# Performance work log

Hardware: AMD Instinct MI355X
Metric: run time of the kernel (lower is better)

The kernel has to match this reference:

```python
import jax, jax.numpy as jnp
import numpy as np

EPS = 1e-12  # F.normalize eps
TEMP = 0.03


def _l2norm(x):
    # torch F.normalize: x / max(||x||, eps)
    n = jnp.sqrt(jnp.sum(x * x, axis=-1, keepdims=True))
    return x / jnp.maximum(n, EPS)


def setup_inputs() -> dict:
    key = jax.random.key(0)
    ks = jax.random.split(key, 8)
    B, C, H, W = 8, 256, 64, 64
    M = 2024
    Ch = C // 4
    s = 1.0 / np.sqrt(C)
    return {
        "feats": jax.random.normal(ks[0], (B, C, H, W), jnp.float32),
        "fg_memory": jax.random.normal(ks[1], (M, C), jnp.float32) * s,
        "bg_memory": jax.random.normal(ks[2], (M, C), jnp.float32) * s,
        "w1_fg": jax.random.normal(ks[3], (C, Ch), jnp.float32) * s,
        "b1_fg": jnp.zeros((Ch,), jnp.float32),
        "w2_fg": jax.random.normal(ks[4], (Ch, 1), jnp.float32) * (1.0 / np.sqrt(Ch)),
        "b2_fg": jnp.zeros((1,), jnp.float32),
        "w1_bg": jax.random.normal(ks[5], (C, Ch), jnp.float32) * s,
        "b1_bg": jnp.zeros((Ch,), jnp.float32),
        "w2_bg": jax.random.normal(ks[6], (Ch, 1), jnp.float32) * (1.0 / np.sqrt(Ch)),
        "b2_bg": jnp.zeros((1,), jnp.float32),
    }


def _gate(x, w1, b1, w2, b2):
    h = jax.nn.relu(x @ w1 + b1)
    return jax.nn.sigmoid(h @ w2 + b2)  # [N,1]


def reference(feats, fg_memory, bg_memory, w1_fg, b1_fg, w2_fg, b2_fg,
              w1_bg, b1_bg, w2_bg, b2_bg):
    B, C, H, W = feats.shape
    x = jnp.transpose(feats, (0, 2, 3, 1)).reshape(-1, C)  # [N,C]
    xn = _l2norm(x)
    fgn = _l2norm(fg_memory)  # [M,C]
    bgn = _l2norm(bg_memory)

    attn_fg = jax.nn.softmax((xn @ fgn.T) / TEMP, axis=1)  # [N,M]
    mem_fg = attn_fg @ fgn                                  # [N,C]
    attn_bg = jax.nn.softmax((xn @ bgn.T) / TEMP, axis=1)
    mem_bg = attn_bg @ bgn

    g_fg = _gate(xn, w1_fg, b1_fg, w2_fg, b2_fg)
    g_bg = _gate(xn, w1_bg, b1_bg, w2_bg, b2_bg)

    fused = xn + g_fg * mem_fg - g_bg * mem_bg
    return jnp.transpose(fused.reshape(B, H, W, C), (0, 3, 1, 2))
```

## Files before the change

kernel.cpp:

```cpp
#include <hip/hip_runtime.h>
#include <math.h>

#define B_   8
#define C_   256
#define HW_  4096
#define N_   32768
#define M_   2024
#define MP_  2048
#define CH_  64
#define NCHUNK (MP_ / 64)
#define INV_TEMP 33.333333333333336f
#define NEPS 1e-12f

typedef __attribute__((ext_vector_type(8))) short short8;
typedef __attribute__((ext_vector_type(4))) float floatx4;

__device__ __forceinline__ float wred64(float s) {
#pragma unroll
  for (int off = 32; off > 0; off >>= 1) s += __shfl_xor(s, off, 64);
  return s;
}

__device__ __forceinline__ unsigned short f2bf(float f) {
  union { float f; unsigned u; } v; v.f = f;
  unsigned r = v.u + 0x7FFFu + ((v.u >> 16) & 1u);
  return (unsigned short)(r >> 16);
}
__device__ __forceinline__ float bf2f(unsigned short b) {
  union { unsigned u; float f; } v; v.u = ((unsigned)b) << 16; return v.f;
}

__device__ __forceinline__ void barrier_lds_only() {
  asm volatile("s_waitcnt lgkmcnt(0)\n\ts_barrier" ::: "memory");
}

__device__ __forceinline__ void async_copy16(const unsigned short* gsrc,
                                             unsigned short* lds) {
  __builtin_amdgcn_global_load_lds(
      (const __attribute__((address_space(1))) void*)gsrc,
      (__attribute__((address_space(3))) void*)lds, 16, 0, 0);
}

__global__ __launch_bounds__(256) void norm_mem_kernel(
    const float* __restrict__ fg, const float* __restrict__ bg,
    unsigned short* __restrict__ fgS, unsigned short* __restrict__ bgS,
    unsigned short* __restrict__ fgT, unsigned short* __restrict__ bgT) {
  __shared__ unsigned short tile[64][258];
  int bid = blockIdx.x;
  const float* src; unsigned short *ms, *mt; int r0;
  if (bid < 32) { src = fg; ms = fgS; mt = fgT; r0 = bid * 64; }
  else          { src = bg; ms = bgS; mt = bgT; r0 = (bid - 32) * 64; }
  int t = threadIdx.x;
  int rr = t >> 2, c4 = t & 3;
  int row = r0 + rr;
  int chunk = r0 >> 6;
  float v[64];
  float s = 0.f;
  if (row < M_) {
    const float4* p = (const float4*)(src + (size_t)row * C_ + c4 * 64);
#pragma unroll
    for (int i = 0; i < 16; ++i) {
      float4 q = p[i];
      v[i * 4 + 0] = q.x; v[i * 4 + 1] = q.y; v[i * 4 + 2] = q.z; v[i * 4 + 3] = q.w;
      s += q.x * q.x + q.y * q.y + q.z * q.z + q.w * q.w;
    }
  } else {
#pragma unroll
    for (int i = 0; i < 64; ++i) v[i] = 0.f;
  }
  s += __shfl_xor(s, 1, 64);
  s += __shfl_xor(s, 2, 64);
  float inv = (row < M_) ? 1.0f / fmaxf(sqrtf(s), NEPS) : 0.f;
#pragma unroll
  for (int i = 0; i < 16; ++i) {
    int c = c4 * 64 + i * 4;
    ushort4 o;
    o.x = f2bf(v[i * 4 + 0] * inv); o.y = f2bf(v[i * 4 + 1] * inv);
    o.z = f2bf(v[i * 4 + 2] * inv); o.w = f2bf(v[i * 4 + 3] * inv);
    int unit = (chunk * 32 + (c >> 5) * 4 + ((c >> 3) & 3)) * 64 + rr;
    *(ushort4*)&ms[(size_t)unit * 8 + (c & 7)] = o;
    *(ushort4*)&tile[rr][c] = o;
  }
  __syncthreads();
  int m = t & 63, cw = t >> 6;
#pragma unroll 8
  for (int j = 0; j < 64; ++j) {
    int c = cw * 64 + j;
    mt[(size_t)c * MP_ + r0 + m] = tile[m][c];
  }
}

__global__ __launch_bounds__(256) void prep_x_kernel(
    const float* __restrict__ feats, float* __restrict__ invn,
    unsigned short* __restrict__ xnb) {
  __shared__ unsigned short tileb[256][66];
  __shared__ float part[4][64];
  __shared__ float invs[64];
  int t = threadIdx.x, hwl = t & 63, cw = t >> 6;
  int n0 = blockIdx.x * 64;
  int b = n0 >> 12, hw0 = n0 & 4095;
  const float* p = feats + (size_t)b * C_ * HW_ + hw0 + hwl;
  float s = 0.f;
#pragma unroll 8
  for (int i = 0; i < 64; ++i) {
    int c = cw * 64 + i;
    float v = p[(size_t)c * HW_];
    s += v * v;
    tileb[c][hwl] = f2bf(v);
  }
  part[cw][hwl] = s;
  __syncthreads();
  if (t < 64) {
    float tot = part[0][t] + part[1][t] + part[2][t] + part[3][t];
    float inv = 1.0f / fmaxf(sqrtf(tot), NEPS);
    invn[n0 + t] = inv;
    invs[t] = inv;
  }
  __syncthreads();
  int px = t >> 2, q = t & 3;
  float iv = invs[px];
  unsigned short* xp = xnb + (size_t)(n0 + px) * C_;
#pragma unroll
  for (int blk = 0; blk < 8; ++blk) {
    int cb = blk * 4 + q;
    short8 o;
#pragma unroll
    for (int j = 0; j < 8; ++j)
      o[j] = (short)f2bf(bf2f(tileb[cb * 8 + j][px]) * iv);
    *(short8*)&xp[cb * 8] = o;
  }
}

__global__ __launch_bounds__(256) void gate_kernel(
    const unsigned short* __restrict__ xnb,
    const float* __restrict__ w1f, const float* __restrict__ b1f,
    const float* __restrict__ w2f, const float* __restrict__ b2f,
    const float* __restrict__ w1b, const float* __restrict__ b1b,
    const float* __restrict__ w2b, const float* __restrict__ b2b,
    float* __restrict__ gf, float* __restrict__ gb) {
  __shared__ float xr[16][C_];
  int t = threadIdx.x, w = t >> 6, lane = t & 63;
  int n0 = blockIdx.x * 16;
#pragma unroll
  for (int pp = 0; pp < 4; ++pp) {
    int px = w * 4 + pp;
    ushort4 u = *(const ushort4*)&xnb[(size_t)(n0 + px) * C_ + lane * 4];
    xr[px][lane * 4 + 0] = bf2f(u.x);
    xr[px][lane * 4 + 1] = bf2f(u.y);
    xr[px][lane * 4 + 2] = bf2f(u.z);
    xr[px][lane * 4 + 3] = bf2f(u.w);
  }
  __syncthreads();
  float hf[4], hb[4];
#pragma unroll
  for (int pp = 0; pp < 4; ++pp) { hf[pp] = b1f[lane]; hb[pp] = b1b[lane]; }
#pragma unroll 4
  for (int c = 0; c < C_; ++c) {
    float wf = w1f[c * CH_ + lane];
    float wb = w1b[c * CH_ + lane];
#pragma unroll
    for (int pp = 0; pp < 4; ++pp) {
      float x = xr[w * 4 + pp][c];
      hf[pp] += x * wf;
      hb[pp] += x * wb;
    }
  }
  float b2fv = b2f[0], b2bv = b2b[0];
#pragma unroll
  for (int pp = 0; pp < 4; ++pp) {
    float sf = fmaxf(hf[pp], 0.f) * w2f[lane];
    float sb = fmaxf(hb[pp], 0.f) * w2b[lane];
    sf = wred64(sf);
    sb = wred64(sb);
    if (lane == 0) {
      gf[n0 + w * 4 + pp] = 1.f / (1.f + __expf(-(sf + b2fv)));
      gb[n0 + w * 4 + pp] = 1.f / (1.f + __expf(-(sb + b2bv)));
    }
  }
}

__device__ __forceinline__ void stage_chunk(const unsigned short* memS, int mc,
                                            unsigned short* mtile, int w, int l) {
  const unsigned short* src = memS + (size_t)mc * 16384;
#pragma unroll
  for (int it = 0; it < 4; ++it) {
    int seg = (it * 8 + w) * 512;
    async_copy16(src + seg + l * 8, mtile + seg);
  }
}

__global__ __launch_bounds__(512, 4) void flash_fused_kernel(
    const unsigned short* __restrict__ xnb,
    const unsigned short* __restrict__ fgS, const unsigned short* __restrict__ fgT,
    const unsigned short* __restrict__ bgS, const unsigned short* __restrict__ bgT,
    const float* __restrict__ gf, const float* __restrict__ gb,
    const float* __restrict__ feats, const float* __restrict__ invn,
    float* __restrict__ out) {
  __shared__ __align__(16) char smem[49664];
  unsigned short* mtile = (unsigned short*)smem;
  unsigned short* Pbuf0 = (unsigned short*)(smem + 32768);
  unsigned short* Pbuf1 = (unsigned short*)(smem + 40960);
  float* rowsum = (float*)(smem + 49152);
  float* comb   = (float*)(smem + 49408);
  float* trans  = (float*)smem;

  int t = threadIdx.x;
  int w = t >> 6, l = t & 63;
  int lm = l & 15, quad = l >> 4;
  int rg = w & 3, mh = w >> 2;
  int row0 = blockIdx.x * 64;

  short8 afrag[8];
  {
    const unsigned short* ap = xnb + (size_t)(row0 + 16 * rg + lm) * C_ + quad * 8;
#pragma unroll
    for (int kb = 0; kb < 8; ++kb)
      afrag[kb] = *(const short8*)(ap + kb * 32);
  }

  int bb = row0 >> 12, hw0 = row0 & 4095;
  float iv = invn[row0 + l];
  size_t ob = (size_t)bb * (size_t)C_ * HW_ + hw0 + l;

#pragma unroll 1
  for (int pass = 0; pass < 2; ++pass) {
    const unsigned short* memS  = pass ? bgS : fgS;
    const unsigned short* membT = pass ? bgT : fgT;
    const float* gp = pass ? gb : gf;

    floatx4 accO[4][2];
#pragma unroll
    for (int rt = 0; rt < 4; ++rt)
#pragma unroll
      for (int ct = 0; ct < 2; ++ct) accO[rt][ct] = (floatx4){0.f, 0.f, 0.f, 0.f};
    float rs[4] = {0.f, 0.f, 0.f, 0.f};
    if (t < 64) rowsum[t] = 0.f;

    stage_chunk(memS, 0, mtile, w, l);

#pragma unroll 1
    for (int mc = 0; mc < NCHUNK; ++mc) {
      __syncthreads();

      short8 bfT[2][2];
#pragma unroll
      for (int ct = 0; ct < 2; ++ct) {
        const unsigned short* tp =
            membT + (size_t)(w * 32 + ct * 16 + lm) * MP_ + mc * 64 + quad * 8;
        bfT[ct][0] = *(const short8*)(tp);
        bfT[ct][1] = *(const short8*)(tp + 32);
      }

      floatx4 accS[2];
      accS[0] = (floatx4){0.f, 0.f, 0.f, 0.f};
      accS[1] = (floatx4){0.f, 0.f, 0.f, 0.f};
      __builtin_amdgcn_s_setprio(1);
#pragma unroll
      for (int mt2 = 0; mt2 < 2; ++mt2) {
        int mrow = mh * 32 + mt2 * 16 + lm;
#pragma unroll
        for (int kb = 0; kb < 8; ++kb) {
          short8 bf = *(const short8*)&mtile[(size_t)(((kb * 4 + quad) * 64) + mrow) * 8];
          accS[mt2] = __builtin_amdgcn_mfma_f32_16x16x32_bf16(afrag[kb], bf, accS[mt2], 0, 0, 0);
        }
      }
      __builtin_amdgcn_s_setprio(0);

      unsigned short* P = (mc & 1) ? Pbuf1 : Pbuf0;
#pragma unroll
      for (int mt2 = 0; mt2 < 2; ++mt2) {
        int m = mh * 32 + mt2 * 16 + lm;
        float ebias = (mc * 64 + m < M_) ? 0.f : -1e30f;
        int g = mh * 4 + mt2 * 2 + (lm >> 3);
#pragma unroll
        for (int r = 0; r < 4; ++r) {
          float pv = __expf(__builtin_fmaf(accS[mt2][r], INV_TEMP, ebias));
          unsigned short pb = f2bf(pv);
          rs[r] += bf2f(pb);
          P[(g * 64 + 16 * rg + quad * 4 + r) * 8 + (lm & 7)] = pb;
        }
      }
      barrier_lds_only();

      if (mc + 1 < NCHUNK) stage_chunk(memS, mc + 1, mtile, w, l);

      __builtin_amdgcn_s_setprio(1);
#pragma unroll
      for (int rt = 0; rt < 4; ++rt) {
        short8 pf0 = *(const short8*)&P[(size_t)((0 + quad) * 64 + rt * 16 + lm) * 8];
        short8 pf1 = *(const short8*)&P[(size_t)((4 + quad) * 64 + rt * 16 + lm) * 8];
#pragma unroll
        for (int ct = 0; ct < 2; ++ct) {
          accO[rt][ct] = __builtin_amdgcn_mfma_f32_16x16x32_bf16(pf0, bfT[ct][0], accO[rt][ct], 0, 0, 0);
          accO[rt][ct] = __builtin_amdgcn_mfma_f32_16x16x32_bf16(pf1, bfT[ct][1], accO[rt][ct], 0, 0, 0);
        }
      }
      __builtin_amdgcn_s_setprio(0);
    }

#pragma unroll
    for (int off = 1; off < 16; off <<= 1)
#pragma unroll
      for (int r = 0; r < 4; ++r) rs[r] += __shfl_xor(rs[r], off, 64);
    if (lm == 0) {
#pragma unroll
      for (int r = 0; r < 4; ++r) atomicAdd(&rowsum[16 * rg + quad * 4 + r], rs[r]);
    }
    __syncthreads();
    if (t < 64) comb[t] = gp[row0 + t] / rowsum[t];
    __syncthreads();

#pragma unroll 1
    for (int cg2 = 0; cg2 < 4; ++cg2) {
      if ((w >> 1) == cg2) {
#pragma unroll
        for (int rt = 0; rt < 4; ++rt)
#pragma unroll
          for (int r = 0; r < 4; ++r) {
            float cf = comb[16 * rt + quad * 4 + r];
#pragma unroll
            for (int ct = 0; ct < 2; ++ct)
              trans[(16 * rt + quad * 4 + r) * 67 + (w & 1) * 32 + ct * 16 + lm] =
                  cf * accO[rt][ct][r];
          }
      }
      __syncthreads();
      if (pass == 0) {
#pragma unroll
        for (int i = 0; i < 8; ++i) {
          int cl = w * 8 + i;
          int cg = cg2 * 64 + cl;
          out[ob + (size_t)cg * HW_] = trans[l * 67 + cl];
        }
      } else {
#pragma unroll
        for (int i = 0; i < 8; ++i) {
          int cl = w * 8 + i;
          int cg = cg2 * 64 + cl;
          size_t a = ob + (size_t)cg * HW_;
          out[a] = feats[a] * iv + out[a] - trans[l * 67 + cl];
        }
      }
      __syncthreads();
    }
  }
}

extern "C" void kernel_launch(void* const* d_in, const int* in_sizes, int n_in,
                              void* d_out, int out_size, void* d_ws, size_t ws_size,
                              hipStream_t stream) {
  const float* feats = (const float*)d_in[0];
  const float* fg    = (const float*)d_in[1];
  const float* bg    = (const float*)d_in[2];
  const float* w1f   = (const float*)d_in[3];
  const float* b1f   = (const float*)d_in[4];
  const float* w2f   = (const float*)d_in[5];
  const float* b2f   = (const float*)d_in[6];
  const float* w1b   = (const float*)d_in[7];
  const float* b1b   = (const float*)d_in[8];
  const float* w2b   = (const float*)d_in[9];
  const float* b2b   = (const float*)d_in[10];
  float* out = (float*)d_out;

  char* ws = (char*)d_ws;
  unsigned short* xnb = (unsigned short*)ws;
  unsigned short* fgS = xnb + (size_t)N_ * C_;
  unsigned short* bgS = fgS + (size_t)MP_ * C_;
  unsigned short* fgT = bgS + (size_t)MP_ * C_;
  unsigned short* bgT = fgT + (size_t)C_ * MP_;
  float* gf   = (float*)(bgT + (size_t)C_ * MP_);
  float* gb   = gf + N_;
  float* invn = gb + N_;

  norm_mem_kernel<<<64, 256, 0, stream>>>(fg, bg, fgS, bgS, fgT, bgT);
  prep_x_kernel<<<N_ / 64, 256, 0, stream>>>(feats, invn, xnb);
  gate_kernel<<<N_ / 16, 256, 0, stream>>>(xnb, w1f, b1f, w2f, b2f,
                                           w1b, b1b, w2b, b2b, gf, gb);
  flash_fused_kernel<<<N_ / 64, 512, 0, stream>>>(
      xnb, fgS, fgT, bgS, bgT, gf, gb, feats, invn, out);
}
```

Before: 350.1 us.

## Fuse gate MLP into flash kernel as extra MFMA chunk of memory tile

The separate gate kernel is removed. The first-layer gate weights (w1) are converted to bf16 and appended as an extra 64-row chunk after each memory bank's staged layout. The flash kernel runs one more chunk iteration per pass that reuses the existing QK^T MFMA path to compute x@w1. That iteration then applies bias, ReLU and the w2 dot product with shuffles and LDS atomics, and the sigmoid is applied at the combine step. This removes one launch and the gate kernel's scalar FMA work and its reread of xn, in exchange for bf16 precision in the gate matmul and one extra loop iteration per pass. The s_setprio hints are also dropped.

```diff
diff --git a/kernel.cpp b/kernel.cpp
--- a/kernel.cpp
+++ b/kernel.cpp
@@ -15,12 +15,6 @@
 typedef __attribute__((ext_vector_type(8))) short short8;
 typedef __attribute__((ext_vector_type(4))) float floatx4;
 
-__device__ __forceinline__ float wred64(float s) {
-#pragma unroll
-  for (int off = 32; off > 0; off >>= 1) s += __shfl_xor(s, off, 64);
-  return s;
-}
-
 __device__ __forceinline__ unsigned short f2bf(float f) {
   union { float f; unsigned u; } v; v.f = f;
   unsigned r = v.u + 0x7FFFu + ((v.u >> 16) & 1u);
@@ -43,15 +37,34 @@
 
 __global__ __launch_bounds__(256) void norm_mem_kernel(
     const float* __restrict__ fg, const float* __restrict__ bg,
+    const float* __restrict__ w1f, const float* __restrict__ w1b,
     unsigned short* __restrict__ fgS, unsigned short* __restrict__ bgS,
     unsigned short* __restrict__ fgT, unsigned short* __restrict__ bgT) {
   __shared__ unsigned short tile[64][258];
   int bid = blockIdx.x;
+  int t = threadIdx.x;
+  int rr = t >> 2, c4 = t & 3;
+
+  if (bid >= 64) {
+    const float* srcw = (bid == 64) ? w1f : w1b;
+    unsigned short* ms = (bid == 64) ? fgS : bgS;
+#pragma unroll
+    for (int i = 0; i < 16; ++i) {
+      int c = c4 * 64 + i * 4;
+      ushort4 o;
+      o.x = f2bf(srcw[(size_t)(c + 0) * CH_ + rr]);
+      o.y = f2bf(srcw[(size_t)(c + 1) * CH_ + rr]);
+      o.z = f2bf(srcw[(size_t)(c + 2) * CH_ + rr]);
+      o.w = f2bf(srcw[(size_t)(c + 3) * CH_ + rr]);
+      int unit = (32 * 32 + (c >> 5) * 4 + ((c >> 3) & 3)) * 64 + rr;
+      *(ushort4*)&ms[(size_t)unit * 8 + (c & 7)] = o;
+    }
+    return;
+  }
+
   const float* src; unsigned short *ms, *mt; int r0;
   if (bid < 32) { src = fg; ms = fgS; mt = fgT; r0 = bid * 64; }
   else          { src = bg; ms = bgS; mt = bgT; r0 = (bid - 32) * 64; }
-  int t = threadIdx.x;
-  int rr = t >> 2, c4 = t & 3;
   int row = r0 + rr;
   int chunk = r0 >> 6;
   float v[64];
@@ -131,54 +144,6 @@
   }
 }
 
-__global__ __launch_bounds__(256) void gate_kernel(
-    const unsigned short* __restrict__ xnb,
-    const float* __restrict__ w1f, const float* __restrict__ b1f,
-    const float* __restrict__ w2f, const float* __restrict__ b2f,
-    const float* __restrict__ w1b, const float* __restrict__ b1b,
-    const float* __restrict__ w2b, const float* __restrict__ b2b,
-    float* __restrict__ gf, float* __restrict__ gb) {
-  __shared__ float xr[16][C_];
-  int t = threadIdx.x, w = t >> 6, lane = t & 63;
-  int n0 = blockIdx.x * 16;
-#pragma unroll
-  for (int pp = 0; pp < 4; ++pp) {
-    int px = w * 4 + pp;
-    ushort4 u = *(const ushort4*)&xnb[(size_t)(n0 + px) * C_ + lane * 4];
-    xr[px][lane * 4 + 0] = bf2f(u.x);
-    xr[px][lane * 4 + 1] = bf2f(u.y);
-    xr[px][lane * 4 + 2] = bf2f(u.z);
-    xr[px][lane * 4 + 3] = bf2f(u.w);
-  }
-  __syncthreads();
-  float hf[4], hb[4];
-#pragma unroll
-  for (int pp = 0; pp < 4; ++pp) { hf[pp] = b1f[lane]; hb[pp] = b1b[lane]; }
-#pragma unroll 4
-  for (int c = 0; c < C_; ++c) {
-    float wf = w1f[c * CH_ + lane];
-    float wb = w1b[c * CH_ + lane];
-#pragma unroll
-    for (int pp = 0; pp < 4; ++pp) {
-      float x = xr[w * 4 + pp][c];
-      hf[pp] += x * wf;
-      hb[pp] += x * wb;
-    }
-  }
-  float b2fv = b2f[0], b2bv = b2b[0];
-#pragma unroll
-  for (int pp = 0; pp < 4; ++pp) {
-    float sf = fmaxf(hf[pp], 0.f) * w2f[lane];
-    float sb = fmaxf(hb[pp], 0.f) * w2b[lane];
-    sf = wred64(sf);
-    sb = wred64(sb);
-    if (lane == 0) {
-      gf[n0 + w * 4 + pp] = 1.f / (1.f + __expf(-(sf + b2fv)));
-      gb[n0 + w * 4 + pp] = 1.f / (1.f + __expf(-(sb + b2bv)));
-    }
-  }
-}
-
 __device__ __forceinline__ void stage_chunk(const unsigned short* memS, int mc,
                                             unsigned short* mtile, int w, int l) {
   const unsigned short* src = memS + (size_t)mc * 16384;
@@ -193,15 +158,18 @@
     const unsigned short* __restrict__ xnb,
     const unsigned short* __restrict__ fgS, const unsigned short* __restrict__ fgT,
     const unsigned short* __restrict__ bgS, const unsigned short* __restrict__ bgT,
-    const float* __restrict__ gf, const float* __restrict__ gb,
     const float* __restrict__ feats, const float* __restrict__ invn,
+    const float* __restrict__ b1fp, const float* __restrict__ w2fp,
+    const float* __restrict__ b2fp, const float* __restrict__ b1bp,
+    const float* __restrict__ w2bp, const float* __restrict__ b2bp,
     float* __restrict__ out) {
-  __shared__ __align__(16) char smem[49664];
+  __shared__ __align__(16) char smem[49920];
   unsigned short* mtile = (unsigned short*)smem;
   unsigned short* Pbuf0 = (unsigned short*)(smem + 32768);
   unsigned short* Pbuf1 = (unsigned short*)(smem + 40960);
   float* rowsum = (float*)(smem + 49152);
   float* comb   = (float*)(smem + 49408);
+  float* gpart  = (float*)(smem + 49664);
   float* trans  = (float*)smem;
 
   int t = threadIdx.x;
@@ -226,7 +194,9 @@
   for (int pass = 0; pass < 2; ++pass) {
     const unsigned short* memS  = pass ? bgS : fgS;
     const unsigned short* membT = pass ? bgT : fgT;
-    const float* gp = pass ? gb : gf;
+    const float* b1p = pass ? b1bp : b1fp;
+    const float* w2p = pass ? w2bp : w2fp;
+    float b2v = (pass ? b2bp : b2fp)[0];
 
     floatx4 accO[4][2];
 #pragma unroll
@@ -234,27 +204,29 @@
 #pragma unroll
       for (int ct = 0; ct < 2; ++ct) accO[rt][ct] = (floatx4){0.f, 0.f, 0.f, 0.f};
     float rs[4] = {0.f, 0.f, 0.f, 0.f};
-    if (t < 64) rowsum[t] = 0.f;
+    if (t < 64) { rowsum[t] = 0.f; gpart[t] = 0.f; }
 
     stage_chunk(memS, 0, mtile, w, l);
 
 #pragma unroll 1
-    for (int mc = 0; mc < NCHUNK; ++mc) {
+    for (int mc = 0; mc <= NCHUNK; ++mc) {
       __syncthreads();
+      bool isGate = (mc == NCHUNK);
 
       short8 bfT[2][2];
-#pragma unroll
-      for (int ct = 0; ct < 2; ++ct) {
-        const unsigned short* tp =
-            membT + (size_t)(w * 32 + ct * 16 + lm) * MP_ + mc * 64 + quad * 8;
-        bfT[ct][0] = *(const short8*)(tp);
-        bfT[ct][1] = *(const short8*)(tp + 32);
+      if (!isGate) {
+#pragma unroll
+        for (int ct = 0; ct < 2; ++ct) {
+          const unsigned short* tp =
+              membT + (size_t)(w * 32 + ct * 16 + lm) * MP_ + mc * 64 + quad * 8;
+          bfT[ct][0] = *(const short8*)(tp);
+          bfT[ct][1] = *(const short8*)(tp + 32);
+        }
       }
 
       floatx4 accS[2];
       accS[0] = (floatx4){0.f, 0.f, 0.f, 0.f};
       accS[1] = (floatx4){0.f, 0.f, 0.f, 0.f};
-      __builtin_amdgcn_s_setprio(1);
 #pragma unroll
       for (int mt2 = 0; mt2 < 2; ++mt2) {
         int mrow = mh * 32 + mt2 * 16 + lm;
@@ -264,38 +236,56 @@
           accS[mt2] = __builtin_amdgcn_mfma_f32_16x16x32_bf16(afrag[kb], bf, accS[mt2], 0, 0, 0);
         }
       }
-      __builtin_amdgcn_s_setprio(0);
-
-      unsigned short* P = (mc & 1) ? Pbuf1 : Pbuf0;
-#pragma unroll
-      for (int mt2 = 0; mt2 < 2; ++mt2) {
-        int m = mh * 32 + mt2 * 16 + lm;
-        float ebias = (mc * 64 + m < M_) ? 0.f : -1e30f;
-        int g = mh * 4 + mt2 * 2 + (lm >> 3);
-#pragma unroll
-        for (int r = 0; r < 4; ++r) {
-          float pv = __expf(__builtin_fmaf(accS[mt2][r], INV_TEMP, ebias));
-          unsigned short pb = f2bf(pv);
-          rs[r] += bf2f(pb);
-          P[(g * 64 + 16 * rg + quad * 4 + r) * 8 + (lm & 7)] = pb;
-        }
-      }
-      barrier_lds_only();
-
-      if (mc + 1 < NCHUNK) stage_chunk(memS, mc + 1, mtile, w, l);
-
-      __builtin_amdgcn_s_setprio(1);
-#pragma unroll
-      for (int rt = 0; rt < 4; ++rt) {
-        short8 pf0 = *(const short8*)&P[(size_t)((0 + quad) * 64 + rt * 16 + lm) * 8];
-        short8 pf1 = *(const short8*)&P[(size_t)((4 + quad) * 64 + rt * 16 + lm) * 8];
-#pragma unroll
-        for (int ct = 0; ct < 2; ++ct) {
-          accO[rt][ct] = __builtin_amdgcn_mfma_f32_16x16x32_bf16(pf0, bfT[ct][0], accO[rt][ct], 0, 0, 0);
-          accO[rt][ct] = __builtin_amdgcn_mfma_f32_16x16x32_bf16(pf1, bfT[ct][1], accO[rt][ct], 0, 0, 0);
-        }
-      }
-      __builtin_amdgcn_s_setprio(0);
+
+      if (!isGate) {
+        unsigned short* P = (mc & 1) ? Pbuf1 : Pbuf0;
+#pragma unroll
+        for (int mt2 = 0; mt2 < 2; ++mt2) {
+          int m = mh * 32 + mt2 * 16 + lm;
+          float ebias = (mc * 64 + m < M_) ? 0.f : -1e30f;
+          int g = mh * 4 + mt2 * 2 + (lm >> 3);
+#pragma unroll
+          for (int r = 0; r < 4; ++r) {
+            float pv = __expf(__builtin_fmaf(accS[mt2][r], INV_TEMP, ebias));
+            unsigned short pb = f2bf(pv);
+            rs[r] += bf2f(pb);
+            P[(g * 64 + 16 * rg + quad * 4 + r) * 8 + (lm & 7)] = pb;
+          }
+        }
+        barrier_lds_only();
+
+        if (mc + 1 <= NCHUNK) stage_chunk(memS, mc + 1, mtile, w, l);
+
+#pragma unroll
+        for (int rt = 0; rt < 4; ++rt) {
+          short8 pf0 = *(const short8*)&P[(size_t)((0 + quad) * 64 + rt * 16 + lm) * 8];
+          short8 pf1 = *(const short8*)&P[(size_t)((4 + quad) * 64 + rt * 16 + lm) * 8];
+#pragma unroll
+          for (int ct = 0; ct < 2; ++ct) {
+            accO[rt][ct] = __builtin_amdgcn_mfma_f32_16x16x32_bf16(pf0, bfT[ct][0], accO[rt][ct], 0, 0, 0);
+            accO[rt][ct] = __builtin_amdgcn_mfma_f32_16x16x32_bf16(pf1, bfT[ct][1], accO[rt][ct], 0, 0, 0);
+          }
+        }
+      } else {
+        float b1a = b1p[mh * 32 + lm];
+        float b1c = b1p[mh * 32 + 16 + lm];
+        float w2a = w2p[mh * 32 + lm];
+        float w2c = w2p[mh * 32 + 16 + lm];
+        float p[4];
+#pragma unroll
+        for (int r = 0; r < 4; ++r)
+          p[r] = fmaxf(accS[0][r] + b1a, 0.f) * w2a +
+                 fmaxf(accS[1][r] + b1c, 0.f) * w2c;
+#pragma unroll
+        for (int off = 1; off < 16; off <<= 1)
+#pragma unroll
+          for (int r = 0; r < 4; ++r) p[r] += __shfl_xor(p[r], off, 64);
+        if (lm == 0) {
+#pragma unroll
+          for (int r = 0; r < 4; ++r)
+            atomicAdd(&gpart[16 * rg + quad * 4 + r], p[r]);
+        }
+      }
     }
 
 #pragma unroll
@@ -307,7 +297,10 @@
       for (int r = 0; r < 4; ++r) atomicAdd(&rowsum[16 * rg + quad * 4 + r], rs[r]);
     }
     __syncthreads();
-    if (t < 64) comb[t] = gp[row0 + t] / rowsum[t];
+    if (t < 64) {
+      float g = 1.f / (1.f + __expf(-(gpart[t] + b2v)));
+      comb[t] = g / rowsum[t];
+    }
     __syncthreads();
 
 #pragma unroll 1
@@ -365,17 +358,14 @@
   char* ws = (char*)d_ws;
   unsigned short* xnb = (unsigned short*)ws;
   unsigned short* fgS = xnb + (size_t)N_ * C_;
-  unsigned short* bgS = fgS + (size_t)MP_ * C_;
-  unsigned short* fgT = bgS + (size_t)MP_ * C_;
+  unsigned short* bgS = fgS + (size_t)(MP_ + 64) * C_;
+  unsigned short* fgT = bgS + (size_t)(MP_ + 64) * C_;
   unsigned short* bgT = fgT + (size_t)C_ * MP_;
-  float* gf   = (float*)(bgT + (size_t)C_ * MP_);
-  float* gb   = gf + N_;
-  float* invn = gb + N_;
-
-  norm_mem_kernel<<<64, 256, 0, stream>>>(fg, bg, fgS, bgS, fgT, bgT);
+  float* invn = (float*)(bgT + (size_t)C_ * MP_);
+
+  norm_mem_kernel<<<66, 256, 0, stream>>>(fg, bg, w1f, w1b, fgS, bgS, fgT, bgT);
   prep_x_kernel<<<N_ / 64, 256, 0, stream>>>(feats, invn, xnb);
-  gate_kernel<<<N_ / 16, 256, 0, stream>>>(xnb, w1f, b1f, w2f, b2f,
-                                           w1b, b1b, w2b, b2b, gf, gb);
   flash_fused_kernel<<<N_ / 64, 512, 0, stream>>>(
-      xnb, fgS, fgT, bgS, bgT, gf, gb, feats, invn, out);
-}
+      xnb, fgS, fgT, bgS, bgT, feats, invn,
+      b1f, w2f, b2f, b1b, w2b, b2b, out);
+}
```

Result: slower. 588.0 us (+67.9%).
